# Optimization experiments

Measured on AMD Instinct MI355X. Metric: run time of the kernel, lower is better.

The kernel has to match this reference:

```python
import jax, jax.numpy as jnp
import numpy as np

B, T, V, E, U = 64, 256, 128, 512, 512


def _lstm_scan(zx, mask_t, Ur, reverse):
    """Masked LSTM over time-major precomputed input projections.
    zx: [T,B,4U] = x@W + b; mask_t: [T,B] bool; Ur: [U,4U].
    Masked steps carry previous h,c (Keras mask semantics).
    reverse=True implements the backward direction of Bidirectional
    (lax.scan reverse keeps outputs aligned with input time order,
    matching Keras' go_backwards + output re-reversal).
    """
    u = Ur.shape[0]
    b = zx.shape[1]

    def step(carry, inp):
        h, c = carry
        zx_t, m = inp
        z = zx_t + h @ Ur
        i, f, g, o = jnp.split(z, 4, axis=-1)
        i = jax.nn.sigmoid(i)
        f = jax.nn.sigmoid(f)
        g = jnp.tanh(g)
        o = jax.nn.sigmoid(o)
        c_new = f * c + i * g
        h_new = o * jnp.tanh(c_new)
        m = m[:, None]
        h_new = jnp.where(m, h_new, h)
        c_new = jnp.where(m, c_new, c)
        return (h_new, c_new), h_new

    init = (jnp.zeros((b, u), zx.dtype), jnp.zeros((b, u), zx.dtype))
    (h, c), ys = jax.lax.scan(step, init, (zx, mask_t), reverse=reverse)
    return ys, h, c


def _bidir_lstm(x, mask_t, Wf, Uf, bf, Wb, Ub, bb):
    # x: [B,T,D] -> time-major [T,B,D]
    xt = jnp.transpose(x, (1, 0, 2))
    ysf, hf, cf = _lstm_scan(xt @ Wf + bf, mask_t, Uf, False)
    ysb, hb, cb = _lstm_scan(xt @ Wb + bb, mask_t, Ub, True)
    ys = jnp.concatenate([ysf, ysb], axis=-1)  # [T,B,2U]
    return (jnp.transpose(ys, (1, 0, 2)),
            jnp.concatenate([hf, hb], axis=-1),
            jnp.concatenate([cf, cb], axis=-1))


def _lstm_params(key, in_dim, units):
    k1, k2, k3 = jax.random.split(key, 3)
    W = jax.random.normal(k1, (in_dim, 4 * units), jnp.float32) / np.sqrt(in_dim)
    Ur = jax.random.normal(k2, (units, 4 * units), jnp.float32) / np.sqrt(units)
    b = jnp.zeros((4 * units,), jnp.float32).at[units:2 * units].set(1.0)  # unit forget bias
    return W, Ur, b


def setup_inputs() -> dict:
    key = jax.random.key(0)
    ks = jax.random.split(key, 6)
    encoder_input = jax.random.randint(ks[0], (B, T), 0, V, dtype=jnp.int32)
    emb = jax.random.normal(ks[1], (V, E), jnp.float32) * 0.05
    W1f, U1f, b1f = _lstm_params(ks[2], E, U)
    W1b, U1b, b1b = _lstm_params(ks[3], E, U)
    W2f, U2f, b2f = _lstm_params(ks[4], 2 * U, U)
    W2b, U2b, b2b = _lstm_params(ks[5], 2 * U, U)
    return {"encoder_input": encoder_input, "emb": emb,
            "W1f": W1f, "U1f": U1f, "b1f": b1f,
            "W1b": W1b, "U1b": U1b, "b1b": b1b,
            "W2f": W2f, "U2f": U2f, "b2f": b2f,
            "W2b": W2b, "U2b": U2b, "b2b": b2b}


def reference(encoder_input, emb, W1f, U1f, b1f, W1b, U1b, b1b,
              W2f, U2f, b2f, W2b, U2b, b2b):
    mask = encoder_input != 0           # [B,T] from mask_zero=True
    mask_t = mask.T                     # [T,B]
    x = emb[encoder_input]              # [B,T,E]
    out1, _h1, _c1 = _bidir_lstm(x, mask_t, W1f, U1f, b1f, W1b, U1b, b1b)
    # dropout is identity at inference (training=False)
    out2, h2, c2 = _bidir_lstm(out1, mask_t, W2f, U2f, b2f, W2b, U2b, b2b)
    return out2, h2, c2
```

## Files before the change

kernel.cpp:

```cpp
#include <hip/hip_runtime.h>

typedef unsigned short u16;
typedef unsigned int u32;
typedef unsigned long long u64;
typedef __attribute__((ext_vector_type(8))) short bf16x8;
typedef __attribute__((ext_vector_type(4))) float f32x4;
typedef __attribute__((ext_vector_type(8))) unsigned short u16x8;
typedef __attribute__((ext_vector_type(4))) unsigned short u16x4;

#define MFMA16(a, b, c) __builtin_amdgcn_mfma_f32_16x16x32_bf16(a, b, c, 0, 0, 0)

__device__ __forceinline__ u16 f2b(float f) {
    u32 u = __builtin_bit_cast(u32, f);
    u32 r = (u + 0x7fffu + ((u >> 16) & 1u)) >> 16;
    return (u16)r;
}
__device__ __forceinline__ float b2f(u16 h) {
    u32 u = ((u32)h) << 16;
    return __builtin_bit_cast(float, u);
}
__device__ __forceinline__ float sigm(float x) { return 1.0f / (1.0f + __expf(-x)); }
__device__ __forceinline__ float tanh_fast(float x) { return 1.0f - 2.0f / (__expf(2.0f * x) + 1.0f); }

__device__ __forceinline__ u32 aload32(const void* p) {
    return __hip_atomic_load((const u32*)p, __ATOMIC_RELAXED, __HIP_MEMORY_SCOPE_AGENT);
}
__device__ __forceinline__ void astore32(void* p, u32 v) {
    __hip_atomic_store((u32*)p, v, __ATOMIC_RELAXED, __HIP_MEMORY_SCOPE_AGENT);
}
__device__ __forceinline__ void astore64(void* p, u64 v) {
    __hip_atomic_store((u64*)p, v, __ATOMIC_RELAXED, __HIP_MEMORY_SCOPE_AGENT);
}

__global__ __launch_bounds__(256) void embed_k(const int* __restrict__ enc,
                                               const float* __restrict__ emb,
                                               u16* __restrict__ xb) {
    int idx = (blockIdx.x * 256 + threadIdx.x) * 4;
    int row = idx >> 9;
    int e = idx & 511;
    int t = row >> 6, b = row & 63;
    int tok = enc[b * 256 + t];
    const float4 v = *(const float4*)(emb + (size_t)tok * 512 + e);
    u16x4 o;
    o.x = f2b(v.x); o.y = f2b(v.y); o.z = f2b(v.z); o.w = f2b(v.w);
    *(u16x4*)(xb + idx) = o;
}

__global__ void mask_k(const int* __restrict__ enc, u64* __restrict__ mw) {
    int t = threadIdx.x;
    u64 m = 0;
#pragma unroll 8
    for (int b = 0; b < 64; ++b)
        if (enc[b * 256 + t] != 0) m |= (1ull << b);
    mw[t] = m;
}

__global__ __launch_bounds__(256) void castT_k(const float* __restrict__ src,
                                               u16* __restrict__ dst, int K, int N) {
    __shared__ float tile[64][65];
    int n0 = blockIdx.x * 64, k0 = blockIdx.y * 64;
    int tid = threadIdx.x;
#pragma unroll
    for (int it = 0; it < 4; ++it) {
        int e = tid + it * 256;
        int kk = e >> 4;
        int nn = (e & 15) * 4;
        const float4 v = *(const float4*)(src + (size_t)(k0 + kk) * N + n0 + nn);
        tile[kk][nn] = v.x; tile[kk][nn + 1] = v.y;
        tile[kk][nn + 2] = v.z; tile[kk][nn + 3] = v.w;
    }
    __syncthreads();
#pragma unroll
    for (int it = 0; it < 2; ++it) {
        int e = tid + it * 256;
        int nn = e >> 3;
        int ks = (e & 7) * 8;
        u16x8 o;
#pragma unroll
        for (int j = 0; j < 8; ++j) o[j] = f2b(tile[ks + j][nn]);
        *(u16x8*)(dst + (size_t)(n0 + nn) * K + k0 + ks) = o;
    }
}

__global__ __launch_bounds__(256) void gemm_bias_k(
    const u16* __restrict__ A, int Ak,
    const u16* __restrict__ BtF, const u16* __restrict__ BtB,
    const float* __restrict__ biasF, const float* __restrict__ biasB,
    u16* __restrict__ outF, u16* __restrict__ outB) {
    const int dir = blockIdx.z;
    const u16* __restrict__ Bt = dir ? BtB : BtF;
    const float* __restrict__ bias = dir ? biasB : biasF;
    u16* __restrict__ out = dir ? outB : outF;

    const int m0 = blockIdx.y * 128, n0 = blockIdx.x * 128;
    __shared__ __align__(16) u16 As[128 * 40];
    __shared__ __align__(16) u16 Bs[128 * 40];
    const int tid = threadIdx.x;
    const int lane = tid & 63, w = tid >> 6;
    const int l15 = lane & 15, quad = lane >> 4;
    const int rb = (w >> 1) * 64, cb = (w & 1) * 64;

    f32x4 acc[4][4];
#pragma unroll
    for (int i = 0; i < 4; ++i)
#pragma unroll
        for (int j = 0; j < 4; ++j) acc[i][j] = (f32x4){0.f, 0.f, 0.f, 0.f};

    const int nkt = Ak >> 5;
    for (int kt = 0; kt < nkt; ++kt) {
        __syncthreads();
#pragma unroll
        for (int it = 0; it < 2; ++it) {
            int s = tid + it * 256;
            int r = s >> 2, seg = s & 3;
            *(uint4*)&As[r * 40 + seg * 8] =
                *(const uint4*)&A[(size_t)(m0 + r) * Ak + kt * 32 + seg * 8];
            *(uint4*)&Bs[r * 40 + seg * 8] =
                *(const uint4*)&Bt[(size_t)(n0 + r) * Ak + kt * 32 + seg * 8];
        }
        __syncthreads();
        bf16x8 af[4], bfr[4];
#pragma unroll
        for (int i = 0; i < 4; ++i)
            af[i] = *(const bf16x8*)&As[(rb + i * 16 + l15) * 40 + quad * 8];
#pragma unroll
        for (int j = 0; j < 4; ++j)
            bfr[j] = *(const bf16x8*)&Bs[(cb + j * 16 + l15) * 40 + quad * 8];
#pragma unroll
        for (int i = 0; i < 4; ++i)
#pragma unroll
            for (int j = 0; j < 4; ++j) acc[i][j] = MFMA16(af[i], bfr[j], acc[i][j]);
    }
#pragma unroll
    for (int j = 0; j < 4; ++j) {
        int col = n0 + cb + j * 16 + l15;
        float bv = bias[col];
#pragma unroll
        for (int i = 0; i < 4; ++i) {
            int m = m0 + rb + i * 16 + quad * 4;
            int t = m >> 6, b0 = m & 63;
            u16x4 o;
#pragma unroll
            for (int r = 0; r < 4; ++r) o[r] = f2b(acc[i][j][r] + bv);
            *(u16x4*)&out[((size_t)t * 2048 + col) * 64 + b0] = o;
        }
    }
}

__global__ __launch_bounds__(256, 1) void lstm_rec_k(
    const u16* __restrict__ zxF, const u16* __restrict__ zxB,
    const u16* __restrict__ UtF, const u16* __restrict__ UtB,
    const u64* __restrict__ maskw,
    u16* __restrict__ hex,
    u32* __restrict__ flgF, u32* __restrict__ flgB,
    float* __restrict__ out2,
    int layer) {
    const int wg = blockIdx.x;
    const int dir = wg >> 6;
    const int wgu = wg & 63;
    const u16* __restrict__ zx = dir ? zxB : zxF;
    const u16* __restrict__ Ut = dir ? UtB : UtF;
    u32* __restrict__ flg = dir ? flgB : flgF;

    const int tid = threadIdx.x;
    const int lane = tid & 63, w = tid >> 6;
    const int l15 = lane & 15, quad = lane >> 4;
    const bool hi = (lane & 8) != 0;
    const int gc_l = (l15 >> 3) * 512 + wgu * 8 + (l15 & 7);
    const int u = wgu * 8 + (lane & 7);
    const int brow = w * 16 + l15;
    const int b0 = w * 16 + quad * 4;

    bf16x8 bfr[2][16];
#pragma unroll
    for (int nt = 0; nt < 2; ++nt)
#pragma unroll
        for (int kt = 0; kt < 16; ++kt)
            bfr[nt][kt] = *(const bf16x8*)&Ut[(size_t)(nt * 1024 + gc_l) * 512 + kt * 32 + quad * 8];

    float hreg[4] = {0.f, 0.f, 0.f, 0.f};
    float creg[4] = {0.f, 0.f, 0.f, 0.f};

    int t0 = dir ? 255 : 0;
    u16x4 pz0 = *(const u16x4*)&zx[((size_t)t0 * 2048 + gc_l) * 64 + b0];
    u16x4 pz1 = *(const u16x4*)&zx[((size_t)t0 * 2048 + 1024 + gc_l) * 64 + b0];

    for (int s = 0; s < 256; ++s) {
        const int t = dir ? (255 - s) : s;
        const int tp = dir ? (t + 1) : (t - 1);

        if (s) {
            if (tid < 64) {
                u32 v = aload32(&flg[tid]);
                while (__ballot(v < (u32)s)) v = aload32(&flg[tid]);
            }
            __syncthreads();
        }

        const u64 mw = maskw[t];

        f32x4 acc0, acc1;
#pragma unroll
        for (int r = 0; r < 4; ++r) { acc0[r] = b2f(pz0[r]); acc1[r] = b2f(pz1[r]); }

        if (s) {
            const u16* hbase = hex + ((size_t)tp * 64 + brow) * 1024 + dir * 512 + quad * 8;
            bf16x8 hfr[16];
#pragma unroll
            for (int kt = 0; kt < 16; ++kt) hfr[kt] = *(const bf16x8*)&hbase[kt * 32];
#pragma unroll
            for (int kt = 0; kt < 16; ++kt) {
                acc0 = MFMA16(hfr[kt], bfr[0][kt], acc0);
                acc1 = MFMA16(hfr[kt], bfr[1][kt], acc1);
            }
        }

#pragma unroll
        for (int r = 0; r < 4; ++r) {
            int b = b0 + r;
            float z0 = acc0[r], z1 = acc1[r];
            float p0 = __shfl_xor(z0, 8);
            float p1 = __shfl_xor(z1, 8);
            float iz = hi ? p0 : z0, fz = hi ? z0 : p0;
            float gz = hi ? p1 : z1, oz = hi ? z1 : p1;
            float i_ = sigm(iz), f_ = sigm(fz), g_ = tanh_fast(gz), o_ = sigm(oz);
            float cn = f_ * creg[r] + i_ * g_;
            float hv = o_ * tanh_fast(cn);
            if (!((mw >> b) & 1ull)) { cn = creg[r]; hv = hreg[r]; }
            creg[r] = cn; hreg[r] = hv;
            if (!hi) {
                u16 hb = f2b(hv);
                u32 pair = (u32)hb | (((u32)(u16)__shfl_xor((int)(u32)hb, 1)) << 16);
                u64 q = (u64)pair | ((u64)(u32)__shfl_xor((int)pair, 2) << 32);
                if (!(lane & 3))
                    astore64(&hex[((size_t)t * 64 + b) * 1024 + dir * 512 + u], q);
            }
        }

        __syncthreads();
        if (tid == 0) astore32(&flg[wgu], (u32)(s + 1));

        if (layer == 2 && !hi) {
#pragma unroll
            for (int r = 0; r < 4; ++r) {
                u32 h32 = __builtin_bit_cast(u32, hreg[r]);
                u32 ot = (u32)__shfl_xor((int)h32, 1);
                if (!(lane & 1)) {
                    u64 qq = (u64)h32 | ((u64)ot << 32);
                    *(u64*)&out2[(size_t)(b0 + r) * 262144 + (size_t)t * 1024 + dir * 512 + u] = qq;
                }
            }
            if (s == 255) {
#pragma unroll
                for (int r = 0; r < 4; ++r) {
                    int b = b0 + r;
                    out2[16777216 + b * 1024 + dir * 512 + u] = hreg[r];
                    out2[16777216 + 65536 + b * 1024 + dir * 512 + u] = creg[r];
                }
            }
        }
        {
            int tn = dir ? (s < 255 ? 254 - s : 0) : (s < 255 ? s + 1 : 255);
            pz0 = *(const u16x4*)&zx[((size_t)tn * 2048 + gc_l) * 64 + b0];
            pz1 = *(const u16x4*)&zx[((size_t)tn * 2048 + 1024 + gc_l) * 64 + b0];
        }
    }
}

extern "C" void kernel_launch(void* const* d_in, const int* in_sizes, int n_in,
                              void* d_out, int out_size, void* d_ws, size_t ws_size,
                              hipStream_t stream) {
    const int* enc = (const int*)d_in[0];
    const float* emb = (const float*)d_in[1];
    const float* W1f = (const float*)d_in[2];
    const float* U1f = (const float*)d_in[3];
    const float* b1f = (const float*)d_in[4];
    const float* W1b = (const float*)d_in[5];
    const float* U1b = (const float*)d_in[6];
    const float* b1b = (const float*)d_in[7];
    const float* W2f = (const float*)d_in[8];
    const float* U2f = (const float*)d_in[9];
    const float* b2f = (const float*)d_in[10];
    const float* W2b = (const float*)d_in[11];
    const float* U2b = (const float*)d_in[12];
    const float* b2b = (const float*)d_in[13];

    char* ws = (char*)d_ws;
    constexpr size_t ZXF = 0;
    constexpr size_t ZXB = 67108864;
    constexpr size_t XB = 134217728;
    constexpr size_t OUT1 = 150994944;
    constexpr size_t WT = 184549376;
    constexpr size_t W1FT = WT + 0;
    constexpr size_t W1BT = WT + 2097152;
    constexpr size_t U1FT = WT + 4194304;
    constexpr size_t U1BT = WT + 6291456;
    constexpr size_t W2FT = WT + 8388608;
    constexpr size_t W2BT = WT + 12582912;
    constexpr size_t U2FT = WT + 16777216;
    constexpr size_t U2BT = WT + 18874368;
    constexpr size_t FLG = 205520896;
    constexpr size_t MASKW = FLG + 4096;

    u16* zxF = (u16*)(ws + ZXF);
    u16* zxB = (u16*)(ws + ZXB);
    u16* xb = (u16*)(ws + XB);
    u16* out1 = (u16*)(ws + OUT1);
    u32* flgs = (u32*)(ws + FLG);
    u64* maskw = (u64*)(ws + MASKW);

    hipMemsetAsync(ws + FLG, 0, 4096, stream);

    embed_k<<<8192, 256, 0, stream>>>(enc, emb, xb);
    mask_k<<<1, 256, 0, stream>>>(enc, maskw);

    castT_k<<<dim3(32, 8), 256, 0, stream>>>(W1f, (u16*)(ws + W1FT), 512, 2048);
    castT_k<<<dim3(32, 8), 256, 0, stream>>>(W1b, (u16*)(ws + W1BT), 512, 2048);
    castT_k<<<dim3(32, 8), 256, 0, stream>>>(U1f, (u16*)(ws + U1FT), 512, 2048);
    castT_k<<<dim3(32, 8), 256, 0, stream>>>(U1b, (u16*)(ws + U1BT), 512, 2048);
    castT_k<<<dim3(32, 16), 256, 0, stream>>>(W2f, (u16*)(ws + W2FT), 1024, 2048);
    castT_k<<<dim3(32, 16), 256, 0, stream>>>(W2b, (u16*)(ws + W2BT), 1024, 2048);
    castT_k<<<dim3(32, 8), 256, 0, stream>>>(U2f, (u16*)(ws + U2FT), 512, 2048);
    castT_k<<<dim3(32, 8), 256, 0, stream>>>(U2b, (u16*)(ws + U2BT), 512, 2048);

    gemm_bias_k<<<dim3(16, 128, 2), 256, 0, stream>>>(
        xb, 512, (u16*)(ws + W1FT), (u16*)(ws + W1BT), b1f, b1b, zxF, zxB);
    lstm_rec_k<<<128, 256, 0, stream>>>(
        zxF, zxB, (u16*)(ws + U1FT), (u16*)(ws + U1BT), maskw,
        out1, &flgs[0], &flgs[64], nullptr, 1);

    gemm_bias_k<<<dim3(16, 128, 2), 256, 0, stream>>>(
        out1, 1024, (u16*)(ws + W2FT), (u16*)(ws + W2BT), b2f, b2b, zxF, zxB);
    hipMemsetAsync(ws + FLG, 0, 4096, stream);
    lstm_rec_k<<<128, 256, 0, stream>>>(
        zxF, zxB, (u16*)(ws + U2FT), (u16*)(ws + U2BT), maskw,
        out1, &flgs[0], &flgs[64], (float*)d_out, 2);
}
```

Measured before the change: 3.122 ms.

## Partition recurrent LSTM workgroups by batch group to shrink inter-block sync

```diff
diff --git a/kernel.cpp b/kernel.cpp
--- a/kernel.cpp
+++ b/kernel.cpp
@@ -139,10 +139,11 @@
         for (int i = 0; i < 4; ++i) {
             int m = m0 + rb + i * 16 + quad * 4;
             int t = m >> 6, b0 = m & 63;
+            int grp = b0 >> 4, bi = b0 & 15;
             u16x4 o;
 #pragma unroll
             for (int r = 0; r < 4; ++r) o[r] = f2b(acc[i][j][r] + bv);
-            *(u16x4*)&out[((size_t)t * 2048 + col) * 64 + b0] = o;
+            *(u16x4*)&out[(((size_t)t * 4 + grp) * 2048 + col) * 16 + bi] = o;
         }
     }
 }
@@ -152,24 +153,26 @@
     const u16* __restrict__ UtF, const u16* __restrict__ UtB,
     const u64* __restrict__ maskw,
     u16* __restrict__ hex,
-    u32* __restrict__ flgF, u32* __restrict__ flgB,
+    u32* __restrict__ flgs,
     float* __restrict__ out2,
     int layer) {
     const int wg = blockIdx.x;
     const int dir = wg >> 6;
-    const int wgu = wg & 63;
+    const int grp = (wg >> 4) & 3;
+    const int wu = wg & 15;
     const u16* __restrict__ zx = dir ? zxB : zxF;
     const u16* __restrict__ Ut = dir ? UtB : UtF;
-    u32* __restrict__ flg = dir ? flgB : flgF;
+    u32* __restrict__ flg = flgs + (dir * 4 + grp) * 32;
 
     const int tid = threadIdx.x;
     const int lane = tid & 63, w = tid >> 6;
     const int l15 = lane & 15, quad = lane >> 4;
     const bool hi = (lane & 8) != 0;
-    const int gc_l = (l15 >> 3) * 512 + wgu * 8 + (l15 & 7);
-    const int u = wgu * 8 + (lane & 7);
-    const int brow = w * 16 + l15;
-    const int b0 = w * 16 + quad * 4;
+    const int gc_l = (l15 >> 3) * 512 + wu * 32 + w * 8 + (l15 & 7);
+    const int u = wu * 32 + w * 8 + (lane & 7);
+    const int brow = grp * 16 + l15;
+    const int b0 = grp * 16 + quad * 4;
+    const int bi0 = quad * 4;
 
     bf16x8 bfr[2][16];
 #pragma unroll
@@ -182,15 +185,15 @@
     float creg[4] = {0.f, 0.f, 0.f, 0.f};
 
     int t0 = dir ? 255 : 0;
-    u16x4 pz0 = *(const u16x4*)&zx[((size_t)t0 * 2048 + gc_l) * 64 + b0];
-    u16x4 pz1 = *(const u16x4*)&zx[((size_t)t0 * 2048 + 1024 + gc_l) * 64 + b0];
+    u16x4 pz0 = *(const u16x4*)&zx[(((size_t)t0 * 4 + grp) * 2048 + gc_l) * 16 + bi0];
+    u16x4 pz1 = *(const u16x4*)&zx[(((size_t)t0 * 4 + grp) * 2048 + 1024 + gc_l) * 16 + bi0];
 
     for (int s = 0; s < 256; ++s) {
         const int t = dir ? (255 - s) : s;
         const int tp = dir ? (t + 1) : (t - 1);
 
         if (s) {
-            if (tid < 64) {
+            if (tid < 16) {
                 u32 v = aload32(&flg[tid]);
                 while (__ballot(v < (u32)s)) v = aload32(&flg[tid]);
             }
@@ -238,7 +241,7 @@
         }
 
         __syncthreads();
-        if (tid == 0) astore32(&flg[wgu], (u32)(s + 1));
+        if (tid == 0) astore32(&flg[wu], (u32)(s + 1));
 
         if (layer == 2 && !hi) {
 #pragma unroll
@@ -261,8 +264,8 @@
         }
         {
             int tn = dir ? (s < 255 ? 254 - s : 0) : (s < 255 ? s + 1 : 255);
-            pz0 = *(const u16x4*)&zx[((size_t)tn * 2048 + gc_l) * 64 + b0];
-            pz1 = *(const u16x4*)&zx[((size_t)tn * 2048 + 1024 + gc_l) * 64 + b0];
+            pz0 = *(const u16x4*)&zx[(((size_t)tn * 4 + grp) * 2048 + gc_l) * 16 + bi0];
+            pz1 = *(const u16x4*)&zx[(((size_t)tn * 4 + grp) * 2048 + 1024 + gc_l) * 16 + bi0];
         }
     }
 }
@@ -327,12 +330,12 @@
         xb, 512, (u16*)(ws + W1FT), (u16*)(ws + W1BT), b1f, b1b, zxF, zxB);
     lstm_rec_k<<<128, 256, 0, stream>>>(
         zxF, zxB, (u16*)(ws + U1FT), (u16*)(ws + U1BT), maskw,
-        out1, &flgs[0], &flgs[64], nullptr, 1);
+        out1, flgs, nullptr, 1);
 
     gemm_bias_k<<<dim3(16, 128, 2), 256, 0, stream>>>(
         out1, 1024, (u16*)(ws + W2FT), (u16*)(ws + W2BT), b2f, b2b, zxF, zxB);
     hipMemsetAsync(ws + FLG, 0, 4096, stream);
     lstm_rec_k<<<128, 256, 0, stream>>>(
         zxF, zxB, (u16*)(ws + U2FT), (u16*)(ws + U2BT), maskw,
-        out1, &flgs[0], &flgs[64], (float*)d_out, 2);
-}
+        out1, flgs, (float*)d_out, 2);
+}
```

After: 2.857 ms. -8.5%, faster.
